# Optimization experiments

Hardware: AMD Instinct MI355X
Metric: run time of the kernel (lower is better)

The kernel has to match this reference:

```python
import jax, jax.numpy as jnp
import numpy as np

N_ITEM_TYPE = 18
N_ITEM_FEAT = 11
N_TYPE_HIDDEN = 32
N_ITEM_HIDDEN = 128
BS, NA, NI = 32, 128, 128


def setup_inputs() -> dict:
    key = jax.random.key(0)
    k1, k2, k3, k4 = jax.random.split(key, 4)
    item_type = jax.random.randint(k1, (BS, NA, NI), 0, N_ITEM_TYPE, dtype=jnp.int64)
    item = jax.random.normal(k2, (BS, NA, NI, N_ITEM_FEAT), dtype=jnp.float32)
    emb = jax.random.normal(k3, (N_ITEM_TYPE, N_TYPE_HIDDEN), dtype=jnp.float32)
    W = jax.random.normal(k4, (N_TYPE_HIDDEN + N_ITEM_FEAT, N_ITEM_HIDDEN), dtype=jnp.float32) * 0.1
    b = jnp.zeros((N_ITEM_HIDDEN,), dtype=jnp.float32)
    return {"item_type": item_type, "item": item, "emb": emb, "W": W, "b": b}


def reference(item_type, item, emb, W, b):
    # embedding gather: [bs, na, ni, 32]
    h_type = emb[item_type]
    # concat features: [bs, na, ni, 43]
    h = jnp.concatenate([h_type, item], axis=-1)
    # Linear + ReLU: [bs, na, ni, n_item_hidden]
    h = jax.nn.relu(jnp.einsum("bnif,fh->bnih", h, W) + b)
    # max-pool over item axis: [bs, na, n_item_hidden]
    return jnp.max(h, axis=2)
```

## Files before the change

### kernel.cpp

```cpp
#include <hip/hip_runtime.h>
#include <hip/hip_bf16.h>
#include <stdint.h>
#include <float.h>


#define NITEM  128
#define NFEAT  11
#define NTH    32
#define NH     128
#define KREAL  43
#define KSTEPS 3
#define SLABDW (NITEM * NFEAT)
#define EMBOFF (12 * 1024)

typedef __attribute__((ext_vector_type(8)))  _Float16 half8;
typedef __attribute__((ext_vector_type(2)))  __fp16   fp16x2;
typedef __attribute__((ext_vector_type(16))) float    f32x16;

union H8 { half8 h8; fp16x2 h2[4]; };

__global__ __launch_bounds__(64) void prep(const float* __restrict__ W,
                                           const float* __restrict__ emb,
                                           _Float16* __restrict__ ws) {
    const int blk  = blockIdx.x;
    const int lane = threadIdx.x;
    if (blk < 12) {
        const int kk  = blk >> 2;
        const int n   = blk & 3;
        const int col = n * 32 + (lane & 31);
        const int k0  = kk * 16 + (lane >> 5) * 8;
        half8 pk;
        #pragma unroll
        for (int q = 0; q < 8; ++q) {
            const int k = k0 + q;
            pk[q] = (_Float16)((k < KREAL) ? W[k * NH + col] : 0.0f);
        }
        ((half8*)ws)[blk * 64 + lane] = pk;
    } else {
        _Float16* eh = ws + EMBOFF / 2;
        #pragma unroll
        for (int j = 0; j < 9; ++j) {
            const int idx = j * 64 + lane;
            eh[idx] = (_Float16)emb[idx];
        }
    }
}

__global__ __launch_bounds__(128, 4) void item_encoder(
    const int*      __restrict__ item_type,
    const float*    __restrict__ item,
    const _Float16* __restrict__ ws,
    const float*    __restrict__ bias,
    float*          __restrict__ out)
{
    __shared__ float slab[SLABDW];

    const int t    = threadIdx.x;
    const int lane = t & 63;
    const int w    = t >> 6;
    const int l31  = lane & 31;
    const int lhi  = lane >> 5;
    const int bn   = blockIdx.x;

    {
        const float4* gsl = (const float4*)(item + (size_t)bn * SLABDW);
        float4*       lsl = (float4*)slab;
        lsl[t]       = gsl[t];
        lsl[t + 128] = gsl[t + 128];
        if (t < 96) lsl[t + 256] = gsl[t + 256];
    }

    int ty[4];
    {
        const int* tb = item_type + (size_t)bn * NITEM + l31;
        #pragma unroll
        for (int rb = 0; rb < 4; ++rb) ty[rb] = tb[rb * 32];
    }

    half8 bf[KSTEPS][2];
    #pragma unroll
    for (int kk = 0; kk < KSTEPS; ++kk)
        #pragma unroll
        for (int n2 = 0; n2 < 2; ++n2)
            bf[kk][n2] = ((const half8*)ws)[(kk * 4 + (w * 2 + n2)) * 64 + lane];

    const _Float16* eh = ws + EMBOFF / 2;
    half8 ea0[4], ea1[4];
    #pragma unroll
    for (int rb = 0; rb < 4; ++rb) {
        const _Float16* eb = eh + ty[rb] * NTH + lhi * 8;
        ea0[rb] = *(const half8*)(eb);
        ea1[rb] = *(const half8*)(eb + 16);
    }

    float bias2[2];
    #pragma unroll
    for (int n2 = 0; n2 < 2; ++n2) bias2[n2] = bias[(w * 2 + n2) * 32 + l31];

    __syncthreads();

    float vm[2] = { -FLT_MAX, -FLT_MAX };

    #pragma unroll
    for (int rb = 0; rb < 4; ++rb) {
        const int r = rb * 32 + l31;

        const float* sp = slab + r * NFEAT;
        float fv[8];
        #pragma unroll
        for (int q = 0; q < 8; ++q) {
            const int  f    = lhi ? ((q < 3) ? 8 + q : 10) : q;
            const bool dead = (lhi && q >= 3);
            const float x = sp[f];
            fv[q] = dead ? 0.0f : x;
        }

        H8 a2;
        a2.h2[0] = __builtin_amdgcn_cvt_pkrtz(fv[0], fv[1]);
        a2.h2[1] = __builtin_amdgcn_cvt_pkrtz(fv[2], fv[3]);
        a2.h2[2] = __builtin_amdgcn_cvt_pkrtz(fv[4], fv[5]);
        a2.h2[3] = __builtin_amdgcn_cvt_pkrtz(fv[6], fv[7]);

        f32x16 acc[2];
        #pragma unroll
        for (int n2 = 0; n2 < 2; ++n2)
            #pragma unroll
            for (int rr = 0; rr < 16; ++rr) acc[n2][rr] = 0.0f;

        #pragma unroll
        for (int n2 = 0; n2 < 2; ++n2) acc[n2] = __builtin_amdgcn_mfma_f32_32x32x16_f16(ea0[rb], bf[0][n2], acc[n2], 0, 0, 0);
        #pragma unroll
        for (int n2 = 0; n2 < 2; ++n2) acc[n2] = __builtin_amdgcn_mfma_f32_32x32x16_f16(ea1[rb], bf[1][n2], acc[n2], 0, 0, 0);
        #pragma unroll
        for (int n2 = 0; n2 < 2; ++n2) acc[n2] = __builtin_amdgcn_mfma_f32_32x32x16_f16(a2.h8,   bf[2][n2], acc[n2], 0, 0, 0);

        #pragma unroll
        for (int n2 = 0; n2 < 2; ++n2) {
            float m = acc[n2][0];
            #pragma unroll
            for (int rr = 1; rr < 16; ++rr) m = fmaxf(m, acc[n2][rr]);
            m = fmaxf(m, __shfl_xor(m, 32));
            vm[n2] = fmaxf(vm[n2], m);
        }
    }

    if (lane < 32) {
        #pragma unroll
        for (int n2 = 0; n2 < 2; ++n2)
            out[(size_t)bn * NH + (w * 2 + n2) * 32 + l31] =
                fmaxf(vm[n2] + bias2[n2], 0.0f);
    }
}

extern "C" void kernel_launch(void* const* d_in, const int* in_sizes, int n_in,
                              void* d_out, int out_size, void* d_ws, size_t ws_size,
                              hipStream_t stream) {
    const int*   item_type = (const int*)  d_in[0];
    const float* item      = (const float*)d_in[1];
    const float* emb       = (const float*)d_in[2];
    const float* W         = (const float*)d_in[3];
    const float* bias      = (const float*)d_in[4];
    float*       out       = (float*)d_out;
    _Float16*    ws        = (_Float16*)d_ws;

    prep<<<13, 64, 0, stream>>>(W, emb, ws);
    item_encoder<<<32 * 128, 128, 0, stream>>>(item_type, item, ws, bias, out);
}
```

Measured before the change: 88.12 us.

## Fuse weight/embedding fp16 prep into main kernel, drop prep launch

Removes the separate prep kernel that converted W and the embedding table to fp16 in workspace. Each block now converts W fragments straight into registers from global fp32, and stages the embedding table as fp16 in padded LDS, gathering from there after the barrier. This saves a kernel launch and the dependency between the two kernels. In exchange every one of the 4096 blocks repeats the conversion work and issues strided scalar W loads.

```diff
diff --git a/kernel.cpp b/kernel.cpp
--- a/kernel.cpp
+++ b/kernel.cpp
@@ -11,7 +11,7 @@
 #define KREAL  43
 #define KSTEPS 3
 #define SLABDW (NITEM * NFEAT)
-#define EMBOFF (12 * 1024)
+#define ESTRIDE 40
 
 typedef __attribute__((ext_vector_type(8)))  _Float16 half8;
 typedef __attribute__((ext_vector_type(2)))  __fp16   fp16x2;
@@ -19,41 +19,16 @@
 
 union H8 { half8 h8; fp16x2 h2[4]; };
 
-__global__ __launch_bounds__(64) void prep(const float* __restrict__ W,
-                                           const float* __restrict__ emb,
-                                           _Float16* __restrict__ ws) {
-    const int blk  = blockIdx.x;
-    const int lane = threadIdx.x;
-    if (blk < 12) {
-        const int kk  = blk >> 2;
-        const int n   = blk & 3;
-        const int col = n * 32 + (lane & 31);
-        const int k0  = kk * 16 + (lane >> 5) * 8;
-        half8 pk;
-        #pragma unroll
-        for (int q = 0; q < 8; ++q) {
-            const int k = k0 + q;
-            pk[q] = (_Float16)((k < KREAL) ? W[k * NH + col] : 0.0f);
-        }
-        ((half8*)ws)[blk * 64 + lane] = pk;
-    } else {
-        _Float16* eh = ws + EMBOFF / 2;
-        #pragma unroll
-        for (int j = 0; j < 9; ++j) {
-            const int idx = j * 64 + lane;
-            eh[idx] = (_Float16)emb[idx];
-        }
-    }
-}
-
 __global__ __launch_bounds__(128, 4) void item_encoder(
-    const int*      __restrict__ item_type,
-    const float*    __restrict__ item,
-    const _Float16* __restrict__ ws,
-    const float*    __restrict__ bias,
-    float*          __restrict__ out)
+    const int*   __restrict__ item_type,
+    const float* __restrict__ item,
+    const float* __restrict__ emb,
+    const float* __restrict__ W,
+    const float* __restrict__ bias,
+    float*       __restrict__ out)
 {
-    __shared__ float slab[SLABDW];
+    __shared__ float    slab[SLABDW];
+    __shared__ _Float16 ehl[18 * ESTRIDE];
 
     const int t    = threadIdx.x;
     const int lane = t & 63;
@@ -70,6 +45,16 @@
         if (t < 96) lsl[t + 256] = gsl[t + 256];
     }
 
+    #pragma unroll
+    for (int j = 0; j < 5; ++j) {
+        const int idx = t + 128 * j;
+        if (idx < 18 * NTH) {
+            const int ety = idx >> 5;
+            const int ec  = idx & 31;
+            ehl[ety * ESTRIDE + ec] = (_Float16)emb[idx];
+        }
+    }
+
     int ty[4];
     {
         const int* tb = item_type + (size_t)bn * NITEM + l31;
@@ -79,18 +64,22 @@
 
     half8 bf[KSTEPS][2];
     #pragma unroll
-    for (int kk = 0; kk < KSTEPS; ++kk)
+    for (int kk = 0; kk < KSTEPS; ++kk) {
         #pragma unroll
-        for (int n2 = 0; n2 < 2; ++n2)
-            bf[kk][n2] = ((const half8*)ws)[(kk * 4 + (w * 2 + n2)) * 64 + lane];
-
-    const _Float16* eh = ws + EMBOFF / 2;
-    half8 ea0[4], ea1[4];
-    #pragma unroll
-    for (int rb = 0; rb < 4; ++rb) {
-        const _Float16* eb = eh + ty[rb] * NTH + lhi * 8;
-        ea0[rb] = *(const half8*)(eb);
-        ea1[rb] = *(const half8*)(eb + 16);
+        for (int n2 = 0; n2 < 2; ++n2) {
+            const int col = (w * 2 + n2) * 32 + l31;
+            const float* wb = W + (kk * 16 + lhi * 8) * NH + col;
+            H8 pk;
+            #pragma unroll
+            for (int qq = 0; qq < 4; ++qq) {
+                const int k0 = kk * 16 + lhi * 8 + 2 * qq;
+                const int k1 = k0 + 1;
+                const float x0 = (k0 < KREAL) ? wb[(2 * qq)     * NH] : 0.0f;
+                const float x1 = (k1 < KREAL) ? wb[(2 * qq + 1) * NH] : 0.0f;
+                pk.h2[qq] = __builtin_amdgcn_cvt_pkrtz(x0, x1);
+            }
+            bf[kk][n2] = pk.h8;
+        }
     }
 
     float bias2[2];
@@ -98,6 +87,14 @@
     for (int n2 = 0; n2 < 2; ++n2) bias2[n2] = bias[(w * 2 + n2) * 32 + l31];
 
     __syncthreads();
+
+    half8 ea0[4], ea1[4];
+    #pragma unroll
+    for (int rb = 0; rb < 4; ++rb) {
+        const _Float16* eb = ehl + ty[rb] * ESTRIDE + lhi * 8;
+        ea0[rb] = *(const half8*)(eb);
+        ea1[rb] = *(const half8*)(eb + 16);
+    }
 
     float vm[2] = { -FLT_MAX, -FLT_MAX };
 
@@ -161,8 +158,6 @@
     const float* W         = (const float*)d_in[3];
     const float* bias      = (const float*)d_in[4];
     float*       out       = (float*)d_out;
-    _Float16*    ws        = (_Float16*)d_ws;
 
-    prep<<<13, 64, 0, stream>>>(W, emb, ws);
-    item_encoder<<<32 * 128, 128, 0, stream>>>(item_type, item, ws, bias, out);
+    item_encoder<<<32 * 128, 128, 0, stream>>>(item_type, item, emb, W, bias, out);
 }
```

Measured after the change: 85.41 us. 3.1% less time.
